# Optimization experiments

Measured on AMD Instinct MI355X. Metric: run time of the kernel, lower is better.

The kernel has to match this reference:

```python
import jax, jax.numpy as jnp
import numpy as np

B, T, D, UNITS = 16, 4096, 1024, 1024


def setup_inputs() -> dict:
    key = jax.random.key(0)
    k1, k2 = jax.random.split(key)
    inputs = jax.random.normal(k1, (B, T, D), dtype=jnp.float32)
    att_keral = jax.random.normal(k2, (UNITS, D), dtype=jnp.float32) * 0.02
    return {"inputs": inputs, "att_keral": att_keral}


def reference(inputs, att_keral):
    # scores[b,t,u] = inputs[b,t,d] * att_keral[u,d] / sqrt(D)
    d = inputs.shape[-1]
    scale = 1.0 / jnp.sqrt(jnp.asarray(d, dtype=jnp.float32))
    scores = jnp.einsum('btd,ud->btu', inputs, att_keral) * scale
    # NOTE: the original computes alpha = softmax(scores) but (for isfinal=False)
    # multiplies the *scaled scores* (not alpha) back with att_keral. We reproduce
    # that exact math (alpha is dead code on this path).
    out = jnp.einsum('btu,ud->btd', scores, att_keral)
    return out
```

## Files before the change

kernel.cpp:

```cpp
#include <hip/hip_runtime.h>


typedef unsigned short u16;
typedef unsigned int u32;
typedef __bf16 bf16x8 __attribute__((ext_vector_type(8)));
typedef float f32x4 __attribute__((ext_vector_type(4)));

#define BAR() __builtin_amdgcn_s_barrier()
#define LGKM0() asm volatile("s_waitcnt lgkmcnt(0)" ::: "memory")
#define VMC(n) asm volatile("s_waitcnt vmcnt(" #n ")" ::: "memory")

__device__ __forceinline__ u16 f2bf(float f) {
  u32 u = __float_as_uint(f);
  u += 0x7fffu + ((u >> 16) & 1u);
  return (u16)(u >> 16);
}

__device__ __forceinline__ void gload_lds16(const void* g, void* l) {
  __builtin_amdgcn_global_load_lds((const __attribute__((address_space(1))) u32*)g,
                                   (__attribute__((address_space(3))) u32*)l,
                                   16, 0, 0);
}

__global__ __launch_bounds__(256) void prep(const float* __restrict__ X,
                                            const float* __restrict__ W,
                                            u16* __restrict__ Xb,
                                            u16* __restrict__ Mb) {
  __shared__ float w1[32][64];
  __shared__ float w2[32][64];
  const int t = threadIdx.x;
  if (blockIdx.x >= 256) {
    const size_t stride = 2048 * 256;
    size_t idx = (size_t)(blockIdx.x - 256) * 256 + t;
#pragma unroll 4
    for (int it = 0; it < 32; ++it, idx += stride) {
      const float4 v = *(const float4*)(X + idx * 4);
      ushort4 d;
      d.x = f2bf(v.x); d.y = f2bf(v.y); d.z = f2bf(v.z); d.w = f2bf(v.w);
      *(ushort4*)(Xb + idx * 4) = d;
    }
    return;
  }
  const int mb = blockIdx.x;
  const int i0 = (mb >> 4) * 64;
  const int j0 = (mb & 15) * 64;
  const int tx = t & 15, ty = t >> 4;
  float acc[4][4] = {};
  for (int u0 = 0; u0 < 1024; u0 += 32) {
    __syncthreads();
#pragma unroll
    for (int p = 0; p < 2; ++p) {
      int idx = p * 256 + t;
      int lu = idx >> 4, lc = (idx & 15) * 4;
      *(float4*)&w1[lu][lc] = *(const float4*)(W + (size_t)(u0 + lu) * 1024 + i0 + lc);
      *(float4*)&w2[lu][lc] = *(const float4*)(W + (size_t)(u0 + lu) * 1024 + j0 + lc);
    }
    __syncthreads();
#pragma unroll 8
    for (int u = 0; u < 32; ++u) {
      float4 a = *(const float4*)&w1[u][ty * 4];
      float4 b = *(const float4*)&w2[u][tx * 4];
      float av[4] = {a.x, a.y, a.z, a.w};
      float bv[4] = {b.x, b.y, b.z, b.w};
#pragma unroll
      for (int e = 0; e < 4; ++e)
#pragma unroll
        for (int f = 0; f < 4; ++f)
          acc[e][f] += av[e] * bv[f];
    }
  }
  const float s = 0.03125f;
#pragma unroll
  for (int e = 0; e < 4; ++e) {
    ushort4 v;
    v.x = f2bf(acc[e][0] * s);
    v.y = f2bf(acc[e][1] * s);
    v.z = f2bf(acc[e][2] * s);
    v.w = f2bf(acc[e][3] * s);
    *(ushort4*)(Mb + (size_t)(i0 + ty * 4 + e) * 1024 + j0 + tx * 4) = v;
  }
}

__global__ __launch_bounds__(512, 2) void gemm8(const u16* __restrict__ Xb,
                                                const u16* __restrict__ Mb,
                                                float* __restrict__ out) {
  __shared__ u16 lA[4][8192];
  __shared__ u16 lB[4][8192];

  const int p = blockIdx.x;
  const int wg = (p & 7) * 128 + (p >> 3);
  const int bm = wg >> 2;
  const int bn = wg & 3;
  const size_t r0 = (size_t)bm * 256;
  const int c0 = bn * 256;

  const int t = threadIdx.x;
  const int lane = t & 63;
  const int w = t >> 6;
  const int wr = w >> 2, wc = w & 3;
  const int fr = lane & 15;
  const int kc = lane >> 4;

  const int srow = t >> 2;
  const int scl = t & 3;
  const int scg = scl ^ ((srow >> 1) & 3);
  const u16* gA0 = Xb + (r0 + srow) * 1024 + scg * 8;
  const u16* gA1 = Xb + (r0 + 128 + srow) * 1024 + scg * 8;
  const u16* gB0 = Mb + (size_t)(c0 + srow) * 1024 + scg * 8;
  const u16* gB1 = Mb + (size_t)(c0 + 128 + srow) * 1024 + scg * 8;
  const int sl0 = w * 512;
  const int sl1 = 4096 + w * 512;

  f32x4 acc[8][4] = {};

#pragma unroll
  for (int jt = 0; jt < 3; ++jt) {
    gload_lds16(gA0 + jt * 32, (void*)&lA[jt][sl0]);
    gload_lds16(gA1 + jt * 32, (void*)&lA[jt][sl1]);
    gload_lds16(gB0 + jt * 32, (void*)&lB[jt][sl0]);
    gload_lds16(gB1 + jt * 32, (void*)&lB[jt][sl1]);
  }
  VMC(8);
  BAR();

  for (int j = 0; j < 32; ++j) {
    const int rb = j & 3;
    const int sb = (j + 3) & 3;
    const u16* bA = &lA[rb][0];
    const u16* bB = &lB[rb][0];
    const int ko = (j + 3) * 32;
    const bool st = (j + 3) < 32;

    bf16x8 af[4], bf[4];
#pragma unroll
    for (int m = 0; m < 4; ++m) {
      const int row = wr * 128 + m * 16 + fr;
      const int cs = kc ^ ((row >> 1) & 3);
      af[m] = *(const bf16x8*)&bA[row * 32 + cs * 8];
    }
#pragma unroll
    for (int n = 0; n < 4; ++n) {
      const int row = wc * 64 + n * 16 + fr;
      const int cs = kc ^ ((row >> 1) & 3);
      bf[n] = *(const bf16x8*)&bB[row * 32 + cs * 8];
    }
    if (st) {
      gload_lds16(gA0 + ko, (void*)&lA[sb][sl0]);
      gload_lds16(gA1 + ko, (void*)&lA[sb][sl1]);
    }
    BAR();
    LGKM0();
    __builtin_amdgcn_s_setprio(1);
#pragma unroll
    for (int m = 0; m < 4; ++m)
#pragma unroll
      for (int n = 0; n < 4; ++n)
        acc[m][n] = __builtin_amdgcn_mfma_f32_16x16x32_bf16(af[m], bf[n],
                                                            acc[m][n], 0, 0, 0);
    __builtin_amdgcn_s_setprio(0);
    BAR();
#pragma unroll
    for (int m = 0; m < 4; ++m) {
      const int row = wr * 128 + (m + 4) * 16 + fr;
      const int cs = kc ^ ((row >> 1) & 3);
      af[m] = *(const bf16x8*)&bA[row * 32 + cs * 8];
    }
    if (st) {
      gload_lds16(gB0 + ko, (void*)&lB[sb][sl0]);
      gload_lds16(gB1 + ko, (void*)&lB[sb][sl1]);
    }
    BAR();
    LGKM0();
    __builtin_amdgcn_s_setprio(1);
#pragma unroll
    for (int m = 0; m < 4; ++m)
#pragma unroll
      for (int n = 0; n < 4; ++n)
        acc[m + 4][n] = __builtin_amdgcn_mfma_f32_16x16x32_bf16(af[m], bf[n],
                                                                acc[m + 4][n], 0, 0, 0);
    __builtin_amdgcn_s_setprio(0);
    if (j < 29) {
      VMC(8);
    } else if (j == 29) {
      VMC(4);
    } else if (j == 30) {
      VMC(0);
    }
    BAR();
  }

  const int ocol = lane & 15;
  const int orow = (lane >> 4) * 4;
#pragma unroll
  for (int m = 0; m < 8; ++m) {
    const size_t rbase = (r0 + wr * 128 + m * 16 + orow) * 1024;
#pragma unroll
    for (int n = 0; n < 4; ++n) {
      float* o = out + rbase + (c0 + wc * 64 + n * 16 + ocol);
      o[0] = acc[m][n][0];
      o[1024] = acc[m][n][1];
      o[2048] = acc[m][n][2];
      o[3072] = acc[m][n][3];
    }
  }
}

__global__ __launch_bounds__(256) void compute_M_fb(const float* __restrict__ W,
                                                    u16* __restrict__ Mb) {
  __shared__ float w1[32][64];
  __shared__ float w2[32][64];
  const int t = threadIdx.x;
  const int i0 = blockIdx.y * 64;
  const int j0 = blockIdx.x * 64;
  const int tx = t & 15, ty = t >> 4;
  float acc[4][4] = {};
  for (int u0 = 0; u0 < 1024; u0 += 32) {
    __syncthreads();
#pragma unroll
    for (int p = 0; p < 2; ++p) {
      int idx = p * 256 + t;
      int lu = idx >> 4, lc = (idx & 15) * 4;
      *(float4*)&w1[lu][lc] = *(const float4*)(W + (size_t)(u0 + lu) * 1024 + i0 + lc);
      *(float4*)&w2[lu][lc] = *(const float4*)(W + (size_t)(u0 + lu) * 1024 + j0 + lc);
    }
    __syncthreads();
#pragma unroll 8
    for (int u = 0; u < 32; ++u) {
      float4 a = *(const float4*)&w1[u][ty * 4];
      float4 b = *(const float4*)&w2[u][tx * 4];
      float av[4] = {a.x, a.y, a.z, a.w};
      float bv[4] = {b.x, b.y, b.z, b.w};
#pragma unroll
      for (int e = 0; e < 4; ++e)
#pragma unroll
        for (int f = 0; f < 4; ++f)
          acc[e][f] += av[e] * bv[f];
    }
  }
  const float s = 0.03125f;
#pragma unroll
  for (int e = 0; e < 4; ++e) {
    ushort4 v;
    v.x = f2bf(acc[e][0] * s);
    v.y = f2bf(acc[e][1] * s);
    v.z = f2bf(acc[e][2] * s);
    v.w = f2bf(acc[e][3] * s);
    *(ushort4*)(Mb + (size_t)(i0 + ty * 4 + e) * 1024 + j0 + tx * 4) = v;
  }
}

__global__ __launch_bounds__(256) void gemm_fused(const float* __restrict__ X,
                                                  const u16* __restrict__ Mb,
                                                  float* __restrict__ out) {
  __shared__ u16 lA[128 * 32];
  __shared__ u16 lB[128 * 32];
  const int p = blockIdx.x;
  const int wg = (p & 7) * 512 + (p >> 3);
  const int bm = wg >> 3;
  const int bn = wg & 7;
  const size_t r0 = (size_t)bm * 128;
  const int c0 = bn * 128;
  const int t = threadIdx.x;
  const int lane = t & 63;
  const int w = t >> 6;
  const int wr = w >> 1, wc = w & 1;
  const int ar_base = t >> 3;
  const int ac = t & 7;
  const int a_chunk = ac >> 1;
  const int a_half = ac & 1;
  const int fr = lane & 15;
  const int kc = lane >> 4;
  f32x4 acc[4][4] = {};
  for (int k0 = 0; k0 < 1024; k0 += 32) {
#pragma unroll
    for (int i = 0; i < 2; ++i) {
      const int slot0 = w * 128 + i * 64;
      const int slot = slot0 + lane;
      const int nr = slot >> 2;
      const int cc = (slot & 3) ^ ((nr >> 1) & 3);
      const char* g = (const char*)(Mb + (size_t)(c0 + nr) * 1024 + k0) + cc * 16;
      gload_lds16(g, (void*)(lB + slot0 * 8));
    }
#pragma unroll
    for (int q = 0; q < 4; ++q) {
      const int ar = q * 32 + ar_base;
      const float4 v = *(const float4*)(X + (r0 + ar) * 1024 + k0 + ac * 4);
      uint2 d;
      d.x = (u32)f2bf(v.x) | ((u32)f2bf(v.y) << 16);
      d.y = (u32)f2bf(v.z) | ((u32)f2bf(v.w) << 16);
      const int cs = a_chunk ^ ((ar >> 1) & 3);
      *(uint2*)&lA[ar * 32 + cs * 8 + a_half * 4] = d;
    }
    __syncthreads();
    bf16x8 afr[4], bfr[4];
#pragma unroll
    for (int m = 0; m < 4; ++m) {
      const int row = wr * 64 + m * 16 + fr;
      const int cs = kc ^ ((row >> 1) & 3);
      afr[m] = *(const bf16x8*)&lA[row * 32 + cs * 8];
    }
#pragma unroll
    for (int n = 0; n < 4; ++n) {
      const int row = wc * 64 + n * 16 + fr;
      const int cs = kc ^ ((row >> 1) & 3);
      bfr[n] = *(const bf16x8*)&lB[row * 32 + cs * 8];
    }
#pragma unroll
    for (int m = 0; m < 4; ++m)
#pragma unroll
      for (int n = 0; n < 4; ++n)
        acc[m][n] = __builtin_amdgcn_mfma_f32_16x16x32_bf16(afr[m], bfr[n],
                                                            acc[m][n], 0, 0, 0);
    __syncthreads();
  }
  const int ocol = lane & 15;
  const int orow = (lane >> 4) * 4;
#pragma unroll
  for (int m = 0; m < 4; ++m) {
    const size_t rbase = (r0 + wr * 64 + m * 16 + orow) * 1024;
#pragma unroll
    for (int n = 0; n < 4; ++n) {
      float* o = out + rbase + (c0 + wc * 64 + n * 16 + ocol);
      o[0] = acc[m][n][0];
      o[1024] = acc[m][n][1];
      o[2048] = acc[m][n][2];
      o[3072] = acc[m][n][3];
    }
  }
}

extern "C" void kernel_launch(void* const* d_in, const int* in_sizes, int n_in,
                              void* d_out, int out_size, void* d_ws, size_t ws_size,
                              hipStream_t stream) {
  const float* X = (const float*)d_in[0];
  const float* W = (const float*)d_in[1];
  float* out = (float*)d_out;
  u16* Mb = (u16*)d_ws;
  u16* Xb = (u16*)((char*)d_ws + (size_t)(1 << 21));

  const size_t need = (size_t)(1 << 21) + (size_t)64 * 1024 * 1024 * 2;
  if (ws_size >= need) {
    prep<<<2304, 256, 0, stream>>>(X, W, Xb, Mb);
    gemm8<<<1024, 512, 0, stream>>>(Xb, Mb, out);
  } else {
    compute_M_fb<<<dim3(16, 16), 256, 0, stream>>>(W, Mb);
    gemm_fused<<<4096, 256, 0, stream>>>(X, Mb, out);
  }
}
```

Baseline: 287.6 us.

## Simplify GEMM main loop to one barrier per k-step and interleave prep blocks

Reworks the bf16 GEMM main loop. Previously it used four barriers per 32-wide k-step, with split A/B loads and half-tile MFMA phases. Now it issues all loads for stage j+2, reads all 8 A fragments and 4 B fragments, runs 32 MFMAs and waits with a single barrier, using a prefetch depth of two stages instead of three. The prep kernel also interleaves its M-computation blocks with the X-conversion blocks (every 9th block), so the slow M blocks are spread across the dispatch rather than front-loaded. The trade-off is less load-ahead slack and more live fragment registers, in exchange for fewer synchronisations.

```diff
diff --git a/kernel.cpp b/kernel.cpp
--- a/kernel.cpp
+++ b/kernel.cpp
@@ -7,8 +7,8 @@
 typedef float f32x4 __attribute__((ext_vector_type(4)));
 
 #define BAR() __builtin_amdgcn_s_barrier()
-#define LGKM0() asm volatile("s_waitcnt lgkmcnt(0)" ::: "memory")
 #define VMC(n) asm volatile("s_waitcnt vmcnt(" #n ")" ::: "memory")
+#define SCHED0() __builtin_amdgcn_sched_barrier(0)
 
 __device__ __forceinline__ u16 f2bf(float f) {
   u32 u = __float_as_uint(f);
@@ -28,10 +28,12 @@
                                             u16* __restrict__ Mb) {
   __shared__ float w1[32][64];
   __shared__ float w2[32][64];
+  const int bid = blockIdx.x;
   const int t = threadIdx.x;
-  if (blockIdx.x >= 256) {
+  if ((bid % 9) != 8) {
+    const int cid = bid - bid / 9;
     const size_t stride = 2048 * 256;
-    size_t idx = (size_t)(blockIdx.x - 256) * 256 + t;
+    size_t idx = (size_t)cid * 256 + t;
 #pragma unroll 4
     for (int it = 0; it < 32; ++it, idx += stride) {
       const float4 v = *(const float4*)(X + idx * 4);
@@ -41,7 +43,7 @@
     }
     return;
   }
-  const int mb = blockIdx.x;
+  const int mb = bid / 9;
   const int i0 = (mb >> 4) * 64;
   const int j0 = (mb & 15) * 64;
   const int tx = t & 15, ty = t >> 4;
@@ -81,9 +83,9 @@
   }
 }
 
-__global__ __launch_bounds__(512, 2) void gemm8(const u16* __restrict__ Xb,
-                                                const u16* __restrict__ Mb,
-                                                float* __restrict__ out) {
+__global__ __launch_bounds__(512, 2) void gemm_pg(const u16* __restrict__ Xb,
+                                                  const u16* __restrict__ Mb,
+                                                  float* __restrict__ out) {
   __shared__ u16 lA[4][8192];
   __shared__ u16 lB[4][8192];
 
@@ -103,89 +105,63 @@
 
   const int srow = t >> 2;
   const int scl = t & 3;
-  const int scg = scl ^ ((srow >> 1) & 3);
-  const u16* gA0 = Xb + (r0 + srow) * 1024 + scg * 8;
-  const u16* gA1 = Xb + (r0 + 128 + srow) * 1024 + scg * 8;
-  const u16* gB0 = Mb + (size_t)(c0 + srow) * 1024 + scg * 8;
-  const u16* gB1 = Mb + (size_t)(c0 + 128 + srow) * 1024 + scg * 8;
-  const int sl0 = w * 512;
-  const int sl1 = 4096 + w * 512;
+  const int csw = scl ^ ((srow >> 1) & 3);
+  const u16* gA  = Xb + (r0 + srow) * 1024 + csw * 8;
+  const u16* gA2 = Xb + (r0 + 128 + srow) * 1024 + csw * 8;
+  const u16* gB  = Mb + (size_t)(c0 + srow) * 1024 + csw * 8;
+  const u16* gB2 = Mb + (size_t)(c0 + 128 + srow) * 1024 + csw * 8;
+  u16* aDst = &lA[0][w * 512];
+  u16* bDst = &lB[0][w * 512];
 
   f32x4 acc[8][4] = {};
 
-#pragma unroll
-  for (int jt = 0; jt < 3; ++jt) {
-    gload_lds16(gA0 + jt * 32, (void*)&lA[jt][sl0]);
-    gload_lds16(gA1 + jt * 32, (void*)&lA[jt][sl1]);
-    gload_lds16(gB0 + jt * 32, (void*)&lB[jt][sl0]);
-    gload_lds16(gB1 + jt * 32, (void*)&lB[jt][sl1]);
-  }
-  VMC(8);
+  gload_lds16(gA, aDst);            gload_lds16(gA2, aDst + 4096);
+  gload_lds16(gB, bDst);            gload_lds16(gB2, bDst + 4096);
+  gload_lds16(gA + 32, aDst + 8192); gload_lds16(gA2 + 32, aDst + 8192 + 4096);
+  gload_lds16(gB + 32, bDst + 8192); gload_lds16(gB2 + 32, bDst + 8192 + 4096);
+  VMC(4);
+  SCHED0();
   BAR();
 
   for (int j = 0; j < 32; ++j) {
-    const int rb = j & 3;
-    const int sb = (j + 3) & 3;
-    const u16* bA = &lA[rb][0];
-    const u16* bB = &lB[rb][0];
-    const int ko = (j + 3) * 32;
-    const bool st = (j + 3) < 32;
-
-    bf16x8 af[4], bf[4];
-#pragma unroll
-    for (int m = 0; m < 4; ++m) {
-      const int row = wr * 128 + m * 16 + fr;
-      const int cs = kc ^ ((row >> 1) & 3);
-      af[m] = *(const bf16x8*)&bA[row * 32 + cs * 8];
-    }
+    const u16* bA = &lA[j & 3][0];
+    const u16* bB = &lB[j & 3][0];
+    const int sb = (j + 2) & 3;
+
+    if (j <= 29) {
+      const int ko = (j + 2) * 32;
+      gload_lds16(gA + ko, aDst + sb * 8192);
+      gload_lds16(gA2 + ko, aDst + sb * 8192 + 4096);
+      gload_lds16(gB + ko, bDst + sb * 8192);
+      gload_lds16(gB2 + ko, bDst + sb * 8192 + 4096);
+    }
+    bf16x8 bf[4], af[8];
 #pragma unroll
     for (int n = 0; n < 4; ++n) {
       const int row = wc * 64 + n * 16 + fr;
       const int cs = kc ^ ((row >> 1) & 3);
       bf[n] = *(const bf16x8*)&bB[row * 32 + cs * 8];
     }
-    if (st) {
-      gload_lds16(gA0 + ko, (void*)&lA[sb][sl0]);
-      gload_lds16(gA1 + ko, (void*)&lA[sb][sl1]);
-    }
-    BAR();
-    LGKM0();
+#pragma unroll
+    for (int m = 0; m < 8; ++m) {
+      const int row = wr * 128 + m * 16 + fr;
+      const int cs = kc ^ ((row >> 1) & 3);
+      af[m] = *(const bf16x8*)&bA[row * 32 + cs * 8];
+    }
     __builtin_amdgcn_s_setprio(1);
 #pragma unroll
-    for (int m = 0; m < 4; ++m)
+    for (int m = 0; m < 8; ++m)
 #pragma unroll
       for (int n = 0; n < 4; ++n)
         acc[m][n] = __builtin_amdgcn_mfma_f32_16x16x32_bf16(af[m], bf[n],
                                                             acc[m][n], 0, 0, 0);
     __builtin_amdgcn_s_setprio(0);
-    BAR();
-#pragma unroll
-    for (int m = 0; m < 4; ++m) {
-      const int row = wr * 128 + (m + 4) * 16 + fr;
-      const int cs = kc ^ ((row >> 1) & 3);
-      af[m] = *(const bf16x8*)&bA[row * 32 + cs * 8];
-    }
-    if (st) {
-      gload_lds16(gB0 + ko, (void*)&lB[sb][sl0]);
-      gload_lds16(gB1 + ko, (void*)&lB[sb][sl1]);
-    }
-    BAR();
-    LGKM0();
-    __builtin_amdgcn_s_setprio(1);
-#pragma unroll
-    for (int m = 0; m < 4; ++m)
-#pragma unroll
-      for (int n = 0; n < 4; ++n)
-        acc[m + 4][n] = __builtin_amdgcn_mfma_f32_16x16x32_bf16(af[m], bf[n],
-                                                                acc[m + 4][n], 0, 0, 0);
-    __builtin_amdgcn_s_setprio(0);
-    if (j < 29) {
-      VMC(8);
-    } else if (j == 29) {
+    if (j <= 29) {
       VMC(4);
     } else if (j == 30) {
       VMC(0);
     }
+    SCHED0();
     BAR();
   }
 
@@ -202,50 +178,6 @@
       o[2048] = acc[m][n][2];
       o[3072] = acc[m][n][3];
     }
-  }
-}
-
-__global__ __launch_bounds__(256) void compute_M_fb(const float* __restrict__ W,
-                                                    u16* __restrict__ Mb) {
-  __shared__ float w1[32][64];
-  __shared__ float w2[32][64];
-  const int t = threadIdx.x;
-  const int i0 = blockIdx.y * 64;
-  const int j0 = blockIdx.x * 64;
-  const int tx = t & 15, ty = t >> 4;
-  float acc[4][4] = {};
-  for (int u0 = 0; u0 < 1024; u0 += 32) {
-    __syncthreads();
-#pragma unroll
-    for (int p = 0; p < 2; ++p) {
-      int idx = p * 256 + t;
-      int lu = idx >> 4, lc = (idx & 15) * 4;
-      *(float4*)&w1[lu][lc] = *(const float4*)(W + (size_t)(u0 + lu) * 1024 + i0 + lc);
-      *(float4*)&w2[lu][lc] = *(const float4*)(W + (size_t)(u0 + lu) * 1024 + j0 + lc);
-    }
-    __syncthreads();
-#pragma unroll 8
-    for (int u = 0; u < 32; ++u) {
-      float4 a = *(const float4*)&w1[u][ty * 4];
-      float4 b = *(const float4*)&w2[u][tx * 4];
-      float av[4] = {a.x, a.y, a.z, a.w};
-      float bv[4] = {b.x, b.y, b.z, b.w};
-#pragma unroll
-      for (int e = 0; e < 4; ++e)
-#pragma unroll
-        for (int f = 0; f < 4; ++f)
-          acc[e][f] += av[e] * bv[f];
-    }
-  }
-  const float s = 0.03125f;
-#pragma unroll
-  for (int e = 0; e < 4; ++e) {
-    ushort4 v;
-    v.x = f2bf(acc[e][0] * s);
-    v.y = f2bf(acc[e][1] * s);
-    v.z = f2bf(acc[e][2] * s);
-    v.w = f2bf(acc[e][3] * s);
-    *(ushort4*)(Mb + (size_t)(i0 + ty * 4 + e) * 1024 + j0 + tx * 4) = v;
   }
 }
 
@@ -329,6 +261,50 @@
   }
 }
 
+__global__ __launch_bounds__(256) void compute_M_fb(const float* __restrict__ W,
+                                                    u16* __restrict__ Mb) {
+  __shared__ float w1[32][64];
+  __shared__ float w2[32][64];
+  const int t = threadIdx.x;
+  const int i0 = blockIdx.y * 64;
+  const int j0 = blockIdx.x * 64;
+  const int tx = t & 15, ty = t >> 4;
+  float acc[4][4] = {};
+  for (int u0 = 0; u0 < 1024; u0 += 32) {
+    __syncthreads();
+#pragma unroll
+    for (int p = 0; p < 2; ++p) {
+      int idx = p * 256 + t;
+      int lu = idx >> 4, lc = (idx & 15) * 4;
+      *(float4*)&w1[lu][lc] = *(const float4*)(W + (size_t)(u0 + lu) * 1024 + i0 + lc);
+      *(float4*)&w2[lu][lc] = *(const float4*)(W + (size_t)(u0 + lu) * 1024 + j0 + lc);
+    }
+    __syncthreads();
+#pragma unroll 8
+    for (int u = 0; u < 32; ++u) {
+      float4 a = *(const float4*)&w1[u][ty * 4];
+      float4 b = *(const float4*)&w2[u][tx * 4];
+      float av[4] = {a.x, a.y, a.z, a.w};
+      float bv[4] = {b.x, b.y, b.z, b.w};
+#pragma unroll
+      for (int e = 0; e < 4; ++e)
+#pragma unroll
+        for (int f = 0; f < 4; ++f)
+          acc[e][f] += av[e] * bv[f];
+    }
+  }
+  const float s = 0.03125f;
+#pragma unroll
+  for (int e = 0; e < 4; ++e) {
+    ushort4 v;
+    v.x = f2bf(acc[e][0] * s);
+    v.y = f2bf(acc[e][1] * s);
+    v.z = f2bf(acc[e][2] * s);
+    v.w = f2bf(acc[e][3] * s);
+    *(ushort4*)(Mb + (size_t)(i0 + ty * 4 + e) * 1024 + j0 + tx * 4) = v;
+  }
+}
+
 extern "C" void kernel_launch(void* const* d_in, const int* in_sizes, int n_in,
                               void* d_out, int out_size, void* d_ws, size_t ws_size,
                               hipStream_t stream) {
@@ -341,7 +317,7 @@
   const size_t need = (size_t)(1 << 21) + (size_t)64 * 1024 * 1024 * 2;
   if (ws_size >= need) {
     prep<<<2304, 256, 0, stream>>>(X, W, Xb, Mb);
-    gemm8<<<1024, 512, 0, stream>>>(Xb, Mb, out);
+    gemm_pg<<<1024, 512, 0, stream>>>(Xb, Mb, out);
   } else {
     compute_M_fb<<<dim3(16, 16), 256, 0, stream>>>(W, Mb);
     gemm_fused<<<4096, 256, 0, stream>>>(X, Mb, out);
```

New measurement: 364.4 us. 1.27x slower.
